# Optimization experiments

Measured on AMD Instinct MI355X. Metric: run time of the kernel, lower is better.

Reference implementation:

```python
import jax, jax.numpy as jnp
import numpy as np

D_MODEL = 1024
NUM_HEADS = 16
D_K = D_MODEL // NUM_HEADS


def setup_inputs() -> dict:
    key = jax.random.key(0)
    ks = jax.random.split(key, 9)
    s = 1.0 / np.sqrt(D_MODEL)
    return {
        "z": jax.random.normal(ks[0], (4, 2048, D_MODEL), dtype=jnp.float32),
        "Wq": jax.random.uniform(ks[1], (D_MODEL, D_MODEL), jnp.float32, -s, s),
        "bq": jax.random.uniform(ks[2], (D_MODEL,), jnp.float32, -s, s),
        "Wk": jax.random.uniform(ks[3], (D_MODEL, D_MODEL), jnp.float32, -s, s),
        "bk": jax.random.uniform(ks[4], (D_MODEL,), jnp.float32, -s, s),
        "Wv": jax.random.uniform(ks[5], (D_MODEL, D_MODEL), jnp.float32, -s, s),
        "bv": jax.random.uniform(ks[6], (D_MODEL,), jnp.float32, -s, s),
        "Wo": jax.random.uniform(ks[7], (D_MODEL, D_MODEL), jnp.float32, -s, s),
        "bo": jax.random.uniform(ks[8], (D_MODEL,), jnp.float32, -s, s),
    }


def reference(z, Wq, bq, Wk, bk, Wv, bv, Wo, bo):
    B, S, _ = z.shape
    # project and split heads: [B, H, S, d_k]
    def proj(W, b):
        return (z @ W.T + b).reshape(B, S, NUM_HEADS, D_K).transpose(0, 2, 1, 3)
    Q, K, V = proj(Wq, bq), proj(Wk, bk), proj(Wv, bv)
    scale = 1.0 / np.sqrt(D_K)
    scores = jnp.einsum('bhqd,bhkd->bhqk', Q, K) * scale
    probs = jax.nn.softmax(scores, axis=-1)
    ctx = jnp.einsum('bhqk,bhkd->bhqd', probs, V)
    ctx = ctx.transpose(0, 2, 1, 3).reshape(B, S, D_MODEL)
    return ctx @ Wo.T + bo
```

## Files before the change

kernel.cpp:

```cpp
#include <hip/hip_runtime.h>
#include <stdint.h>

#define D_MODEL 1024
#define NHEAD 16
#define DKH 64
#define BATCH 4
#define SEQ 2048
#define M_ROWS (BATCH*SEQ)
#define NBH (BATCH*NHEAD)

typedef float f32x4 __attribute__((ext_vector_type(4)));
typedef float f32x16 __attribute__((ext_vector_type(16)));
typedef __bf16 bf16x8 __attribute__((ext_vector_type(8)));
typedef __bf16 bf16x4v __attribute__((ext_vector_type(4)));
typedef short short4v __attribute__((ext_vector_type(4)));
typedef unsigned int uint2v __attribute__((ext_vector_type(2)));

__device__ __forceinline__ unsigned short f2bf(float x) {
    __bf16 b = (__bf16)x;
    return __builtin_bit_cast(unsigned short, b);
}

#define GLL(gsrc, ldst) \
    __builtin_amdgcn_global_load_lds((const __attribute__((address_space(1))) void*)(gsrc), \
                                     (__attribute__((address_space(3))) void*)(ldst), 16, 0, 0)

__global__ __launch_bounds__(256) void k_convert(
    const float* __restrict__ z,  const float* __restrict__ wq,
    const float* __restrict__ wk, const float* __restrict__ wv,
    const float* __restrict__ wo,
    const float* __restrict__ bq, const float* __restrict__ bk,
    const float* __restrict__ bv,
    unsigned short* __restrict__ zb, unsigned short* __restrict__ wqkv,
    unsigned short* __restrict__ wob, float* __restrict__ biasf)
{
    int i = blockIdx.x * 256 + threadIdx.x;
    {
        float4 v = ((const float4*)z)[i];
        ushort4 o; o.x = f2bf(v.x); o.y = f2bf(v.y); o.z = f2bf(v.z); o.w = f2bf(v.w);
        ((ushort4*)zb)[i] = o;
    }
    if (i < 262144) {
        float4 v;
        ushort4 o;
        v = ((const float4*)wq)[i];
        o.x=f2bf(v.x); o.y=f2bf(v.y); o.z=f2bf(v.z); o.w=f2bf(v.w);
        ((ushort4*)wqkv)[i] = o;
        v = ((const float4*)wk)[i];
        o.x=f2bf(v.x); o.y=f2bf(v.y); o.z=f2bf(v.z); o.w=f2bf(v.w);
        ((ushort4*)wqkv)[262144 + i] = o;
        v = ((const float4*)wv)[i];
        o.x=f2bf(v.x); o.y=f2bf(v.y); o.z=f2bf(v.z); o.w=f2bf(v.w);
        ((ushort4*)wqkv)[524288 + i] = o;
        v = ((const float4*)wo)[i];
        o.x=f2bf(v.x); o.y=f2bf(v.y); o.z=f2bf(v.z); o.w=f2bf(v.w);
        ((ushort4*)wob)[i] = o;
    }
    if (i < 1024) {
        biasf[i]        = bq[i];
        biasf[1024 + i] = bk[i];
        biasf[2048 + i] = bv[i];
    }
}

__global__ __launch_bounds__(256) void k_gemm_qkv(
    const unsigned short* __restrict__ A,
    const unsigned short* __restrict__ Bw,
    const float* __restrict__ biasf,
    unsigned short* __restrict__ qb, unsigned short* __restrict__ kb,
    unsigned short* __restrict__ vtb)
{
    __shared__ unsigned short lds_a[128 * 32];
    __shared__ unsigned short lds_b[128 * 32];

    const int NT = 3072 / 128;
    int bid = blockIdx.x;
    int tn = bid % NT, tm = bid / NT;
    int m0 = tm * 128, n0 = tn * 128;
    int tid = threadIdx.x, wid = tid >> 6, lane = tid & 63;
    int wm = wid >> 1, wn = wid & 1;

    f32x4 acc[4][4] = {};

    int srow = lane >> 2;
    int scol = (lane & 3) * 8;

    for (int kt = 0; kt < 32; ++kt) {
        int k0 = kt * 32;
#pragma unroll
        for (int i = 0; i < 2; ++i) {
            int rb = (wid * 2 + i) * 16;
            GLL(A  + (size_t)(m0 + rb + srow) * 1024 + k0 + scol, lds_a + rb * 32);
            GLL(Bw + (size_t)(n0 + rb + srow) * 1024 + k0 + scol, lds_b + rb * 32);
        }
        __syncthreads();
        bf16x8 af[4], bfr[4];
#pragma unroll
        for (int i = 0; i < 4; ++i)
            af[i] = *(const bf16x8*)(lds_a + (wm * 64 + i * 16 + (lane & 15)) * 32 + (lane >> 4) * 8);
#pragma unroll
        for (int j = 0; j < 4; ++j)
            bfr[j] = *(const bf16x8*)(lds_b + (wn * 64 + j * 16 + (lane & 15)) * 32 + (lane >> 4) * 8);
#pragma unroll
        for (int i = 0; i < 4; ++i)
#pragma unroll
            for (int j = 0; j < 4; ++j)
                acc[i][j] = __builtin_amdgcn_mfma_f32_16x16x32_bf16(af[i], bfr[j], acc[i][j], 0, 0, 0);
        __syncthreads();
    }

    const float QSC = 0.18033688011112042f;
    int t = n0 >> 10;
#pragma unroll
    for (int j = 0; j < 4; ++j) {
        int col = n0 + wn * 64 + j * 16 + (lane & 15);
        float bias = biasf[col];
        int d  = col & 1023;
        int h  = d >> 6;
        int dk = d & 63;
#pragma unroll
        for (int i = 0; i < 4; ++i) {
#pragma unroll
            for (int r = 0; r < 4; ++r) {
                int row = m0 + wm * 64 + i * 16 + (lane >> 4) * 4 + r;
                float v = acc[i][j][r] + bias;
                if (t == 0) v *= QSC;
                unsigned short bv16 = f2bf(v);
                int b_ = row >> 11, s_ = row & 2047;
                int bh = b_ * NHEAD + h;
                if (t == 0) {
                    qb[((size_t)bh * SEQ + s_) * DKH + dk] = bv16;
                } else if (t == 1) {
                    int kvblk = s_ >> 6, r64 = s_ & 63;
                    int t32 = r64 >> 5, l5 = r64 & 31;
                    int ds = dk >> 4, hi2 = (dk >> 3) & 1, e = dk & 7;
                    kb[((size_t)(bh * 32 + kvblk)) * 4096 +
                       (t32 * 4 + ds) * 512 + (hi2 * 32 + l5) * 8 + e] = bv16;
                } else {
                    int kvblk = s_ >> 6, kv64 = s_ & 63;
                    int ks = kv64 >> 3, hi2 = (kv64 >> 2) & 1, e = kv64 & 3;
                    int vt = dk >> 5, l5 = dk & 31;
                    vtb[((size_t)(bh * 32 + kvblk)) * 4096 +
                        (vt * 8 + ks) * 256 + (hi2 * 32 + l5) * 4 + e] = bv16;
                }
            }
        }
    }
}


#define ATTN_STEP(LDSK, LDSV, WPREV, WCUR, DO_PV)                                   \
    {                                                                               \
        f32x16 st0 = {}, st1 = {};                                                  \
        __builtin_amdgcn_s_setprio(1);                                              \
        _Pragma("unroll")                                                           \
        for (int ds = 0; ds < 4; ++ds) {                                            \
            bf16x8 kf0 = *(const bf16x8*)(&(LDSK)[(ds) * 512 + lane * 8]);          \
            bf16x8 kf1 = *(const bf16x8*)(&(LDSK)[(4 + ds) * 512 + lane * 8]);      \
            st0 = __builtin_amdgcn_mfma_f32_32x32x16_bf16(kf0, aq[ds], st0, 0, 0, 0); \
            st1 = __builtin_amdgcn_mfma_f32_32x32x16_bf16(kf1, aq[ds], st1, 0, 0, 0); \
            if (DO_PV) {                                                            \
                short4v vf0 = *(const short4v*)(&(LDSV)[(2 * ds) * 256 + lane * 4]);        \
                short4v vf1 = *(const short4v*)(&(LDSV)[(8 + 2 * ds) * 256 + lane * 4]);    \
                oa0 = __builtin_amdgcn_mfma_f32_32x32x8bf16_1k(vf0, WPREV[2 * ds], oa0, 0, 0, 0); \
                oa1 = __builtin_amdgcn_mfma_f32_32x32x8bf16_1k(vf1, WPREV[2 * ds], oa1, 0, 0, 0); \
                short4v vf2 = *(const short4v*)(&(LDSV)[(2 * ds + 1) * 256 + lane * 4]);    \
                short4v vf3 = *(const short4v*)(&(LDSV)[(8 + 2 * ds + 1) * 256 + lane * 4]);\
                oa0 = __builtin_amdgcn_mfma_f32_32x32x8bf16_1k(vf2, WPREV[2 * ds + 1], oa0, 0, 0, 0); \
                oa1 = __builtin_amdgcn_mfma_f32_32x32x8bf16_1k(vf3, WPREV[2 * ds + 1], oa1, 0, 0, 0); \
            }                                                                       \
        }                                                                           \
        __builtin_amdgcn_s_setprio(0);                                              \
        _Pragma("unroll")                                                           \
        for (int ks = 0; ks < 4; ++ks) {                                            \
            {                                                                       \
                float p0 = __builtin_amdgcn_exp2f(st0[4 * ks + 0]);                 \
                float p1 = __builtin_amdgcn_exp2f(st0[4 * ks + 1]);                 \
                float p2 = __builtin_amdgcn_exp2f(st0[4 * ks + 2]);                 \
                float p3 = __builtin_amdgcn_exp2f(st0[4 * ks + 3]);                 \
                lsum += (p0 + p1) + (p2 + p3);                                      \
                bf16x4v pb;                                                         \
                pb[0] = (__bf16)p0; pb[1] = (__bf16)p1; pb[2] = (__bf16)p2; pb[3] = (__bf16)p3; \
                WCUR[ks] = __builtin_bit_cast(short4v, pb);                         \
            }                                                                       \
            {                                                                       \
                float p0 = __builtin_amdgcn_exp2f(st1[4 * ks + 0]);                 \
                float p1 = __builtin_amdgcn_exp2f(st1[4 * ks + 1]);                 \
                float p2 = __builtin_amdgcn_exp2f(st1[4 * ks + 2]);                 \
                float p3 = __builtin_amdgcn_exp2f(st1[4 * ks + 3]);                 \
                lsum += (p0 + p1) + (p2 + p3);                                      \
                bf16x4v pb;                                                         \
                pb[0] = (__bf16)p0; pb[1] = (__bf16)p1; pb[2] = (__bf16)p2; pb[3] = (__bf16)p3; \
                WCUR[4 + ks] = __builtin_bit_cast(short4v, pb);                     \
            }                                                                       \
        }                                                                           \
    }

#define DRAIN_BARRIER()                                         \
    asm volatile("s_waitcnt vmcnt(0)" ::: "memory");            \
    __builtin_amdgcn_sched_barrier(0);                          \
    __builtin_amdgcn_s_barrier();

__global__ __launch_bounds__(512) void k_attn(
    const unsigned short* __restrict__ qg,
    const unsigned short* __restrict__ kb,
    const unsigned short* __restrict__ vtb,
    unsigned short* __restrict__ ctxb)
{
    __shared__ unsigned short lds_k[2][4096];
    __shared__ unsigned short lds_v[2][4096];

    int bid = blockIdx.x;
    int x = bid & 7, li = bid >> 3;
    int bh = x * 8 + (li >> 3);
    int qt = li & 7;

    int tid = threadIdx.x, wid = tid >> 6, lane = tid & 63;
    int lq = lane & 31, hi = lane >> 5;

    bf16x8 aq[4];
    {
        const unsigned short* qp = qg + ((size_t)bh * SEQ + qt * 256 + wid * 32 + lq) * DKH + hi * 8;
#pragma unroll
        for (int d = 0; d < 4; ++d) aq[d] = *(const bf16x8*)(qp + d * 16);
    }

    float lsum = 0.f;
    f32x16 oa0 = {};
    f32x16 oa1 = {};
    short4v wA[8], wB[8];

    const unsigned short* kbase = kb  + (size_t)bh * 32 * 4096;
    const unsigned short* vbase = vtb + (size_t)bh * 32 * 4096;
    int so = wid * 512 + lane * 8;
    unsigned short* ldk0 = &lds_k[0][wid * 512];
    unsigned short* ldk1 = &lds_k[1][wid * 512];
    unsigned short* ldv0 = &lds_v[0][wid * 512];
    unsigned short* ldv1 = &lds_v[1][wid * 512];

    GLL(kbase + so, ldk0);
    DRAIN_BARRIER();

    GLL(kbase + 4096 + so, ldk1);
    GLL(vbase + so, ldv0);
    ATTN_STEP(lds_k[0], lds_v[0], wB, wA, false);
    DRAIN_BARRIER();

    for (int t = 1; t < 31; t += 2) {
        GLL(kbase + (size_t)(t + 1) * 4096 + so, ldk0);
        GLL(vbase + (size_t)t * 4096 + so, ldv1);
        ATTN_STEP(lds_k[1], lds_v[0], wA, wB, true);
        DRAIN_BARRIER();
        if (t + 2 < 32) GLL(kbase + (size_t)(t + 2) * 4096 + so, ldk1);
        GLL(vbase + (size_t)(t + 1) * 4096 + so, ldv0);
        ATTN_STEP(lds_k[0], lds_v[1], wB, wA, true);
        DRAIN_BARRIER();
    }

    GLL(vbase + (size_t)31 * 4096 + so, ldv1);
    ATTN_STEP(lds_k[1], lds_v[0], wA, wB, true);
    DRAIN_BARRIER();

    __builtin_amdgcn_s_setprio(1);
#pragma unroll
    for (int ks = 0; ks < 8; ++ks) {
        short4v vf0 = *(const short4v*)(&lds_v[1][(ks) * 256 + lane * 4]);
        short4v vf1 = *(const short4v*)(&lds_v[1][(8 + ks) * 256 + lane * 4]);
        oa0 = __builtin_amdgcn_mfma_f32_32x32x8bf16_1k(vf0, wB[ks], oa0, 0, 0, 0);
        oa1 = __builtin_amdgcn_mfma_f32_32x32x8bf16_1k(vf1, wB[ks], oa1, 0, 0, 0);
    }
    __builtin_amdgcn_s_setprio(0);

    int b_ = bh >> 4, h = bh & 15;
    lsum += __shfl_xor(lsum, 32);
    float inv = 1.0f / lsum;
    int s_ = qt * 256 + wid * 32 + lq;
    unsigned short* op = ctxb + (((size_t)b_ * SEQ + s_) * NHEAD + h) * DKH;
#pragma unroll
    for (int m = 0; m < 4; ++m) {
        {
            unsigned int u0 = ((unsigned int)f2bf(oa0[4 * m + 1] * inv) << 16) | f2bf(oa0[4 * m + 0] * inv);
            unsigned int u1 = ((unsigned int)f2bf(oa0[4 * m + 3] * inv) << 16) | f2bf(oa0[4 * m + 2] * inv);
            *(uint2v*)(op + 8 * m + 4 * hi) = (uint2v){ u0, u1 };
        }
        {
            unsigned int u0 = ((unsigned int)f2bf(oa1[4 * m + 1] * inv) << 16) | f2bf(oa1[4 * m + 0] * inv);
            unsigned int u1 = ((unsigned int)f2bf(oa1[4 * m + 3] * inv) << 16) | f2bf(oa1[4 * m + 2] * inv);
            *(uint2v*)(op + 32 + 8 * m + 4 * hi) = (uint2v){ u0, u1 };
        }
    }
}

__global__ __launch_bounds__(256) void k_gemm_out(
    const unsigned short* __restrict__ A,
    const unsigned short* __restrict__ Bw,
    const float* __restrict__ bo,
    float* __restrict__ out)
{
    __shared__ unsigned short lds_a[128 * 32];
    __shared__ unsigned short lds_b[128 * 32];

    const int NT = 1024 / 128;
    int bid = blockIdx.x;
    int tn = bid % NT, tm = bid / NT;
    int m0 = tm * 128, n0 = tn * 128;
    int tid = threadIdx.x, wid = tid >> 6, lane = tid & 63;
    int wm = wid >> 1, wn = wid & 1;

    f32x4 acc[4][4] = {};

    int srow = lane >> 2;
    int scol = (lane & 3) * 8;

    for (int kt = 0; kt < 32; ++kt) {
        int k0 = kt * 32;
#pragma unroll
        for (int i = 0; i < 2; ++i) {
            int rb = (wid * 2 + i) * 16;
            GLL(A  + (size_t)(m0 + rb + srow) * 1024 + k0 + scol, lds_a + rb * 32);
            GLL(Bw + (size_t)(n0 + rb + srow) * 1024 + k0 + scol, lds_b + rb * 32);
        }
        __syncthreads();
        bf16x8 af[4], bfr[4];
#pragma unroll
        for (int i = 0; i < 4; ++i)
            af[i] = *(const bf16x8*)(lds_a + (wm * 64 + i * 16 + (lane & 15)) * 32 + (lane >> 4) * 8);
#pragma unroll
        for (int j = 0; j < 4; ++j)
            bfr[j] = *(const bf16x8*)(lds_b + (wn * 64 + j * 16 + (lane & 15)) * 32 + (lane >> 4) * 8);
#pragma unroll
        for (int i = 0; i < 4; ++i)
#pragma unroll
            for (int j = 0; j < 4; ++j)
                acc[i][j] = __builtin_amdgcn_mfma_f32_16x16x32_bf16(af[i], bfr[j], acc[i][j], 0, 0, 0);
        __syncthreads();
    }

#pragma unroll
    for (int j = 0; j < 4; ++j) {
        int col = n0 + wn * 64 + j * 16 + (lane & 15);
        float bias = bo[col];
#pragma unroll
        for (int i = 0; i < 4; ++i) {
#pragma unroll
            for (int r = 0; r < 4; ++r) {
                int row = m0 + wm * 64 + i * 16 + (lane >> 4) * 4 + r;
                out[(size_t)row * 1024 + col] = acc[i][j][r] + bias;
            }
        }
    }
}

extern "C" void kernel_launch(void* const* d_in, const int* in_sizes, int n_in,
                              void* d_out, int out_size, void* d_ws, size_t ws_size,
                              hipStream_t stream)
{
    const float* z  = (const float*)d_in[0];
    const float* Wq = (const float*)d_in[1];
    const float* bq = (const float*)d_in[2];
    const float* Wk = (const float*)d_in[3];
    const float* bk = (const float*)d_in[4];
    const float* Wv = (const float*)d_in[5];
    const float* bv = (const float*)d_in[6];
    const float* Wo = (const float*)d_in[7];
    const float* bo = (const float*)d_in[8];
    float* out = (float*)d_out;

    char* ws = (char*)d_ws;
    unsigned short* zb   = (unsigned short*)(ws);
    unsigned short* ctxb = (unsigned short*)(ws);
    unsigned short* wqkv = (unsigned short*)(ws + (16ull << 20));
    unsigned short* wob  = (unsigned short*)(ws + (22ull << 20));
    float*          biasf= (float*)(ws + (24ull << 20));
    unsigned short* qb   = (unsigned short*)(ws + (25ull << 20));
    unsigned short* kb   = (unsigned short*)(ws + (41ull << 20));
    unsigned short* vtb  = (unsigned short*)(ws + (57ull << 20));

    k_convert<<<8192, 256, 0, stream>>>(z, Wq, Wk, Wv, Wo, bq, bk, bv, zb, wqkv, wob, biasf);
    k_gemm_qkv<<<64 * 24, 256, 0, stream>>>(zb, wqkv, biasf, qb, kb, vtb);
    k_attn<<<NBH * 8, 512, 0, stream>>>(qb, kb, vtb, ctxb);
    k_gemm_out<<<64 * 8, 256, 0, stream>>>(ctxb, wob, bo, out);
}
```

Measured before the change: 223.3 us.

## Rewrite GEMMs with fragment-packed operands, 256x128 tiles and triple-buffered LDS pipeline

The convert kernel now writes z, the QKV weights and Wo in an MFMA-fragment-ordered layout, and the attention kernel writes its context output in the same layout. Both GEMMs switch to 512-thread blocks with 256x128 tiles and K-steps of 64. They use a three-stage LDS ring fed by global_load_lds with explicit vmcnt waits, plus a block-index swizzle for L2 locality. The goal is to hide global-load latency, drop a barrier per step and raise MFMA density, at the cost of more LDS (144KB) and therefore lower occupancy.

```diff
diff --git a/kernel.cpp b/kernel.cpp
--- a/kernel.cpp
+++ b/kernel.cpp
@@ -14,6 +14,8 @@
 typedef __bf16 bf16x8 __attribute__((ext_vector_type(8)));
 typedef __bf16 bf16x4v __attribute__((ext_vector_type(4)));
 typedef short short4v __attribute__((ext_vector_type(4)));
+typedef unsigned short ushort4v __attribute__((ext_vector_type(4)));
+typedef unsigned short ushort8v __attribute__((ext_vector_type(8)));
 typedef unsigned int uint2v __attribute__((ext_vector_type(2)));
 
 __device__ __forceinline__ unsigned short f2bf(float x) {
@@ -24,6 +26,17 @@
 #define GLL(gsrc, ldst) \
     __builtin_amdgcn_global_load_lds((const __attribute__((address_space(1))) void*)(gsrc), \
                                      (__attribute__((address_space(3))) void*)(ldst), 16, 0, 0)
+
+
+__device__ __forceinline__ void cvt8store(const float* __restrict__ src,
+                                          unsigned short* __restrict__ dst) {
+    float4 v0 = *(const float4*)(src);
+    float4 v1 = *(const float4*)(src + 4);
+    ushort8v o;
+    o[0] = f2bf(v0.x); o[1] = f2bf(v0.y); o[2] = f2bf(v0.z); o[3] = f2bf(v0.w);
+    o[4] = f2bf(v1.x); o[5] = f2bf(v1.y); o[6] = f2bf(v1.z); o[7] = f2bf(v1.w);
+    *(ushort8v*)dst = o;
+}
 
 __global__ __launch_bounds__(256) void k_convert(
     const float* __restrict__ z,  const float* __restrict__ wq,
@@ -31,30 +44,36 @@
     const float* __restrict__ wo,
     const float* __restrict__ bq, const float* __restrict__ bk,
     const float* __restrict__ bv,
-    unsigned short* __restrict__ zb, unsigned short* __restrict__ wqkv,
-    unsigned short* __restrict__ wob, float* __restrict__ biasf)
+    unsigned short* __restrict__ zf, unsigned short* __restrict__ wqkvf,
+    unsigned short* __restrict__ wobf, float* __restrict__ biasf)
 {
     int i = blockIdx.x * 256 + threadIdx.x;
-    {
-        float4 v = ((const float4*)z)[i];
-        ushort4 o; o.x = f2bf(v.x); o.y = f2bf(v.y); o.z = f2bf(v.z); o.w = f2bf(v.w);
-        ((ushort4*)zb)[i] = o;
-    }
-    if (i < 262144) {
-        float4 v;
-        ushort4 o;
-        v = ((const float4*)wq)[i];
-        o.x=f2bf(v.x); o.y=f2bf(v.y); o.z=f2bf(v.z); o.w=f2bf(v.w);
-        ((ushort4*)wqkv)[i] = o;
-        v = ((const float4*)wk)[i];
-        o.x=f2bf(v.x); o.y=f2bf(v.y); o.z=f2bf(v.z); o.w=f2bf(v.w);
-        ((ushort4*)wqkv)[262144 + i] = o;
-        v = ((const float4*)wv)[i];
-        o.x=f2bf(v.x); o.y=f2bf(v.y); o.z=f2bf(v.z); o.w=f2bf(v.w);
-        ((ushort4*)wqkv)[524288 + i] = o;
-        v = ((const float4*)wo)[i];
-        o.x=f2bf(v.x); o.y=f2bf(v.y); o.z=f2bf(v.z); o.w=f2bf(v.w);
-        ((ushort4*)wob)[i] = o;
+    if (i < 1048576) {
+        int lane = i & 63, rest = i >> 6;
+        int kk = rest & 1, mfrag = (rest >> 1) & 7, half = (rest >> 4) & 1;
+        int kt = (rest >> 5) & 15, mtile = rest >> 9;
+        int row = mtile * 256 + half * 128 + mfrag * 16 + (lane & 15);
+        int k = kt * 64 + kk * 32 + (lane >> 4) * 8;
+        cvt8store(z + (size_t)row * 1024 + k, zf + (size_t)i * 8);
+    }
+    int i2 = i - 1048576;
+    if (i2 >= 0 && i2 < 393216) {
+        int lane = i2 & 63, rest = i2 >> 6;
+        int kk = rest & 1, nfrag = (rest >> 1) & 7;
+        int kt = (rest >> 4) & 15, ntile = rest >> 8;
+        int n = ntile * 128 + nfrag * 16 + (lane & 15);
+        int k = kt * 64 + kk * 32 + (lane >> 4) * 8;
+        const float* W = (n < 1024) ? wq : ((n < 2048) ? wk : wv);
+        cvt8store(W + (size_t)(n & 1023) * 1024 + k, wqkvf + (size_t)i2 * 8);
+    }
+    int i3 = i2 - 393216;
+    if (i3 >= 0 && i3 < 131072) {
+        int lane = i3 & 63, rest = i3 >> 6;
+        int kk = rest & 1, nfrag = (rest >> 1) & 7;
+        int kt = (rest >> 4) & 15, ntile = rest >> 8;
+        int n = ntile * 128 + nfrag * 16 + (lane & 15);
+        int k = kt * 64 + kk * 32 + (lane >> 4) * 8;
+        cvt8store(wo + (size_t)n * 1024 + k, wobf + (size_t)i3 * 8);
     }
     if (i < 1024) {
         biasf[i]        = bq[i];
@@ -63,91 +82,107 @@
     }
 }
 
-__global__ __launch_bounds__(256) void k_gemm_qkv(
-    const unsigned short* __restrict__ A,
-    const unsigned short* __restrict__ Bw,
+__device__ __forceinline__ void g_stage(const unsigned short* __restrict__ as_,
+                                        const unsigned short* __restrict__ bs_,
+                                        unsigned short* la, unsigned short* lb,
+                                        int wid, int lane)
+{
+#pragma unroll
+    for (int g = 0; g < 4; ++g)
+        GLL(as_ + (wid + 8 * g) * 512 + lane * 8, la + (wid + 8 * g) * 512);
+#pragma unroll
+    for (int g = 0; g < 2; ++g)
+        GLL(bs_ + (wid + 8 * g) * 512 + lane * 8, lb + (wid + 8 * g) * 512);
+}
+
+#define GEMM_KLOOP(Abase, Bbase)                                                      \
+    g_stage(Abase, Bbase, &ldsA[0][0], &ldsB[0][0], wid, lane);                       \
+    g_stage(Abase + 16384, Bbase + 8192, &ldsA[1][0], &ldsB[1][0], wid, lane);        \
+    asm volatile("s_waitcnt vmcnt(6)" ::: "memory");                                  \
+    __builtin_amdgcn_s_barrier();                                                     \
+    for (int t = 0; t < 16; ++t) {                                                    \
+        int buf = t % 3;                                                              \
+        if (t + 2 < 16)                                                               \
+            g_stage(Abase + (size_t)(t + 2) * 16384, Bbase + (size_t)(t + 2) * 8192,  \
+                    &ldsA[(t + 2) % 3][0], &ldsB[(t + 2) % 3][0], wid, lane);         \
+        const unsigned short* A = &ldsA[buf][0];                                      \
+        const unsigned short* B = &ldsB[buf][0];                                      \
+        bf16x8 b00 = *(const bf16x8*)(B + ((wn * 2 + 0) * 2 + 0) * 512 + lane * 8);   \
+        bf16x8 b01 = *(const bf16x8*)(B + ((wn * 2 + 0) * 2 + 1) * 512 + lane * 8);   \
+        bf16x8 b10 = *(const bf16x8*)(B + ((wn * 2 + 1) * 2 + 0) * 512 + lane * 8);   \
+        bf16x8 b11 = *(const bf16x8*)(B + ((wn * 2 + 1) * 2 + 1) * 512 + lane * 8);   \
+        _Pragma("unroll")                                                             \
+        for (int ii = 0; ii < 8; ++ii) {                                              \
+            bf16x8 a0 = *(const bf16x8*)(A + ((wm * 8 + ii) * 2 + 0) * 512 + lane * 8); \
+            bf16x8 a1 = *(const bf16x8*)(A + ((wm * 8 + ii) * 2 + 1) * 512 + lane * 8); \
+            acc[ii][0] = __builtin_amdgcn_mfma_f32_16x16x32_bf16(a0, b00, acc[ii][0], 0, 0, 0); \
+            acc[ii][0] = __builtin_amdgcn_mfma_f32_16x16x32_bf16(a1, b01, acc[ii][0], 0, 0, 0); \
+            acc[ii][1] = __builtin_amdgcn_mfma_f32_16x16x32_bf16(a0, b10, acc[ii][1], 0, 0, 0); \
+            acc[ii][1] = __builtin_amdgcn_mfma_f32_16x16x32_bf16(a1, b11, acc[ii][1], 0, 0, 0); \
+        }                                                                             \
+        if (t < 14)       { asm volatile("s_waitcnt vmcnt(6)" ::: "memory"); }        \
+        else if (t == 14) { asm volatile("s_waitcnt vmcnt(0)" ::: "memory"); }        \
+        if (t < 15) { __builtin_amdgcn_sched_barrier(0); __builtin_amdgcn_s_barrier(); } \
+    }
+
+__global__ __launch_bounds__(512) void k_gemm_qkv(
+    const unsigned short* __restrict__ Af,
+    const unsigned short* __restrict__ Bf,
     const float* __restrict__ biasf,
-    unsigned short* __restrict__ qb, unsigned short* __restrict__ kb,
-    unsigned short* __restrict__ vtb)
-{
-    __shared__ unsigned short lds_a[128 * 32];
-    __shared__ unsigned short lds_b[128 * 32];
-
-    const int NT = 3072 / 128;
+    unsigned short* __restrict__ qb, unsigned short* __restrict__ kfrag,
+    unsigned short* __restrict__ vfrag)
+{
+    __shared__ unsigned short ldsA[3][16384];
+    __shared__ unsigned short ldsB[3][8192];
+
     int bid = blockIdx.x;
-    int tn = bid % NT, tm = bid / NT;
-    int m0 = tm * 128, n0 = tn * 128;
+    int wg = (bid & 7) * 96 + (bid >> 3);
+    int tn = wg % 24, tm = wg / 24;
     int tid = threadIdx.x, wid = tid >> 6, lane = tid & 63;
-    int wm = wid >> 1, wn = wid & 1;
-
-    f32x4 acc[4][4] = {};
-
-    int srow = lane >> 2;
-    int scol = (lane & 3) * 8;
-
-    for (int kt = 0; kt < 32; ++kt) {
-        int k0 = kt * 32;
-#pragma unroll
-        for (int i = 0; i < 2; ++i) {
-            int rb = (wid * 2 + i) * 16;
-            GLL(A  + (size_t)(m0 + rb + srow) * 1024 + k0 + scol, lds_a + rb * 32);
-            GLL(Bw + (size_t)(n0 + rb + srow) * 1024 + k0 + scol, lds_b + rb * 32);
-        }
-        __syncthreads();
-        bf16x8 af[4], bfr[4];
-#pragma unroll
-        for (int i = 0; i < 4; ++i)
-            af[i] = *(const bf16x8*)(lds_a + (wm * 64 + i * 16 + (lane & 15)) * 32 + (lane >> 4) * 8);
-#pragma unroll
-        for (int j = 0; j < 4; ++j)
-            bfr[j] = *(const bf16x8*)(lds_b + (wn * 64 + j * 16 + (lane & 15)) * 32 + (lane >> 4) * 8);
-#pragma unroll
-        for (int i = 0; i < 4; ++i)
-#pragma unroll
-            for (int j = 0; j < 4; ++j)
-                acc[i][j] = __builtin_amdgcn_mfma_f32_16x16x32_bf16(af[i], bfr[j], acc[i][j], 0, 0, 0);
-        __syncthreads();
-    }
+    int wm = wid >> 2, wn = wid & 3;
+
+    const unsigned short* Abase = Af + (size_t)tm * 16 * 16384;
+    const unsigned short* Bbase = Bf + (size_t)tn * 16 * 8192;
+
+    f32x4 acc[8][2] = {};
+    GEMM_KLOOP(Abase, Bbase)
 
     const float QSC = 0.18033688011112042f;
-    int t = n0 >> 10;
-#pragma unroll
-    for (int j = 0; j < 4; ++j) {
-        int col = n0 + wn * 64 + j * 16 + (lane & 15);
+    int t3 = tn >> 3;
+#pragma unroll
+    for (int j = 0; j < 2; ++j) {
+        int col = tn * 128 + wn * 32 + j * 16 + (lane & 15);
         float bias = biasf[col];
-        int d  = col & 1023;
-        int h  = d >> 6;
-        int dk = d & 63;
-#pragma unroll
-        for (int i = 0; i < 4; ++i) {
+        int d = col & 1023, h = d >> 6, dk = d & 63;
+#pragma unroll
+        for (int i = 0; i < 8; ++i) {
 #pragma unroll
             for (int r = 0; r < 4; ++r) {
-                int row = m0 + wm * 64 + i * 16 + (lane >> 4) * 4 + r;
+                int row = tm * 256 + wm * 128 + i * 16 + (lane >> 4) * 4 + r;
                 float v = acc[i][j][r] + bias;
-                if (t == 0) v *= QSC;
+                if (t3 == 0) v *= QSC;
                 unsigned short bv16 = f2bf(v);
                 int b_ = row >> 11, s_ = row & 2047;
                 int bh = b_ * NHEAD + h;
-                if (t == 0) {
+                if (t3 == 0) {
                     qb[((size_t)bh * SEQ + s_) * DKH + dk] = bv16;
-                } else if (t == 1) {
+                } else if (t3 == 1) {
                     int kvblk = s_ >> 6, r64 = s_ & 63;
                     int t32 = r64 >> 5, l5 = r64 & 31;
                     int ds = dk >> 4, hi2 = (dk >> 3) & 1, e = dk & 7;
-                    kb[((size_t)(bh * 32 + kvblk)) * 4096 +
-                       (t32 * 4 + ds) * 512 + (hi2 * 32 + l5) * 8 + e] = bv16;
+                    kfrag[((size_t)(bh * 32 + kvblk)) * 4096 +
+                          (t32 * 4 + ds) * 512 + (hi2 * 32 + l5) * 8 + e] = bv16;
                 } else {
                     int kvblk = s_ >> 6, kv64 = s_ & 63;
                     int ks = kv64 >> 3, hi2 = (kv64 >> 2) & 1, e = kv64 & 3;
                     int vt = dk >> 5, l5 = dk & 31;
-                    vtb[((size_t)(bh * 32 + kvblk)) * 4096 +
-                        (vt * 8 + ks) * 256 + (hi2 * 32 + l5) * 4 + e] = bv16;
+                    vfrag[((size_t)(bh * 32 + kvblk)) * 4096 +
+                          (vt * 8 + ks) * 256 + (hi2 * 32 + l5) * 4 + e] = bv16;
                 }
             }
         }
     }
 }
-
 
 #define ATTN_STEP(LDSK, LDSV, WPREV, WCUR, DO_PV)                                   \
     {                                                                               \
@@ -205,7 +240,7 @@
     const unsigned short* __restrict__ qg,
     const unsigned short* __restrict__ kb,
     const unsigned short* __restrict__ vtb,
-    unsigned short* __restrict__ ctxb)
+    unsigned short* __restrict__ ctxf)
 {
     __shared__ unsigned short lds_k[2][4096];
     __shared__ unsigned short lds_v[2][4096];
@@ -275,76 +310,52 @@
     lsum += __shfl_xor(lsum, 32);
     float inv = 1.0f / lsum;
     int s_ = qt * 256 + wid * 32 + lq;
-    unsigned short* op = ctxb + (((size_t)b_ * SEQ + s_) * NHEAD + h) * DKH;
+    int row = b_ * 2048 + s_;
+    int mtile = row >> 8, half = (row >> 7) & 1, mfrag = (row >> 4) & 7, lrow = row & 15;
+    unsigned short* cb = ctxf + (size_t)((mtile * 16 + h) * 2 + half) * 8192
+                              + mfrag * 1024 + lrow * 8 + 4 * hi;
 #pragma unroll
     for (int m = 0; m < 4; ++m) {
-        {
-            unsigned int u0 = ((unsigned int)f2bf(oa0[4 * m + 1] * inv) << 16) | f2bf(oa0[4 * m + 0] * inv);
-            unsigned int u1 = ((unsigned int)f2bf(oa0[4 * m + 3] * inv) << 16) | f2bf(oa0[4 * m + 2] * inv);
-            *(uint2v*)(op + 8 * m + 4 * hi) = (uint2v){ u0, u1 };
-        }
-        {
-            unsigned int u0 = ((unsigned int)f2bf(oa1[4 * m + 1] * inv) << 16) | f2bf(oa1[4 * m + 0] * inv);
-            unsigned int u1 = ((unsigned int)f2bf(oa1[4 * m + 3] * inv) << 16) | f2bf(oa1[4 * m + 2] * inv);
-            *(uint2v*)(op + 32 + 8 * m + 4 * hi) = (uint2v){ u0, u1 };
-        }
-    }
-}
-
-__global__ __launch_bounds__(256) void k_gemm_out(
-    const unsigned short* __restrict__ A,
-    const unsigned short* __restrict__ Bw,
+        ushort4v s0, s1;
+        s0[0] = f2bf(oa0[4 * m + 0] * inv); s0[1] = f2bf(oa0[4 * m + 1] * inv);
+        s0[2] = f2bf(oa0[4 * m + 2] * inv); s0[3] = f2bf(oa0[4 * m + 3] * inv);
+        *(ushort4v*)(cb + m * 128) = s0;
+        s1[0] = f2bf(oa1[4 * m + 0] * inv); s1[1] = f2bf(oa1[4 * m + 1] * inv);
+        s1[2] = f2bf(oa1[4 * m + 2] * inv); s1[3] = f2bf(oa1[4 * m + 3] * inv);
+        *(ushort4v*)(cb + 512 + m * 128) = s1;
+    }
+}
+
+__global__ __launch_bounds__(512) void k_gemm_out(
+    const unsigned short* __restrict__ Af,
+    const unsigned short* __restrict__ Bf,
     const float* __restrict__ bo,
     float* __restrict__ out)
 {
-    __shared__ unsigned short lds_a[128 * 32];
-    __shared__ unsigned short lds_b[128 * 32];
-
-    const int NT = 1024 / 128;
+    __shared__ unsigned short ldsA[3][16384];
+    __shared__ unsigned short ldsB[3][8192];
+
     int bid = blockIdx.x;
-    int tn = bid % NT, tm = bid / NT;
-    int m0 = tm * 128, n0 = tn * 128;
+    int wg = (bid & 7) * 32 + (bid >> 3);
+    int tn = wg % 8, tm = wg / 8;
     int tid = threadIdx.x, wid = tid >> 6, lane = tid & 63;
-    int wm = wid >> 1, wn = wid & 1;
-
-    f32x4 acc[4][4] = {};
-
-    int srow = lane >> 2;
-    int scol = (lane & 3) * 8;
-
-    for (int kt = 0; kt < 32; ++kt) {
-        int k0 = kt * 32;
-#pragma unroll
-        for (int i = 0; i < 2; ++i) {
-            int rb = (wid * 2 + i) * 16;
-            GLL(A  + (size_t)(m0 + rb + srow) * 1024 + k0 + scol, lds_a + rb * 32);
-            GLL(Bw + (size_t)(n0 + rb + srow) * 1024 + k0 + scol, lds_b + rb * 32);
-        }
-        __syncthreads();
-        bf16x8 af[4], bfr[4];
-#pragma unroll
-        for (int i = 0; i < 4; ++i)
-            af[i] = *(const bf16x8*)(lds_a + (wm * 64 + i * 16 + (lane & 15)) * 32 + (lane >> 4) * 8);
-#pragma unroll
-        for (int j = 0; j < 4; ++j)
-            bfr[j] = *(const bf16x8*)(lds_b + (wn * 64 + j * 16 + (lane & 15)) * 32 + (lane >> 4) * 8);
-#pragma unroll
-        for (int i = 0; i < 4; ++i)
-#pragma unroll
-            for (int j = 0; j < 4; ++j)
-                acc[i][j] = __builtin_amdgcn_mfma_f32_16x16x32_bf16(af[i], bfr[j], acc[i][j], 0, 0, 0);
-        __syncthreads();
-    }
-
-#pragma unroll
-    for (int j = 0; j < 4; ++j) {
-        int col = n0 + wn * 64 + j * 16 + (lane & 15);
+    int wm = wid >> 2, wn = wid & 3;
+
+    const unsigned short* Abase = Af + (size_t)tm * 16 * 16384;
+    const unsigned short* Bbase = Bf + (size_t)tn * 16 * 8192;
+
+    f32x4 acc[8][2] = {};
+    GEMM_KLOOP(Abase, Bbase)
+
+#pragma unroll
+    for (int j = 0; j < 2; ++j) {
+        int col = tn * 128 + wn * 32 + j * 16 + (lane & 15);
         float bias = bo[col];
 #pragma unroll
-        for (int i = 0; i < 4; ++i) {
+        for (int i = 0; i < 8; ++i) {
 #pragma unroll
             for (int r = 0; r < 4; ++r) {
-                int row = m0 + wm * 64 + i * 16 + (lane >> 4) * 4 + r;
+                int row = tm * 256 + wm * 128 + i * 16 + (lane >> 4) * 4 + r;
                 out[(size_t)row * 1024 + col] = acc[i][j][r] + bias;
             }
         }
@@ -367,17 +378,17 @@
     float* out = (float*)d_out;
 
     char* ws = (char*)d_ws;
-    unsigned short* zb   = (unsigned short*)(ws);
-    unsigned short* ctxb = (unsigned short*)(ws);
-    unsigned short* wqkv = (unsigned short*)(ws + (16ull << 20));
-    unsigned short* wob  = (unsigned short*)(ws + (22ull << 20));
-    float*          biasf= (float*)(ws + (24ull << 20));
-    unsigned short* qb   = (unsigned short*)(ws + (25ull << 20));
-    unsigned short* kb   = (unsigned short*)(ws + (41ull << 20));
-    unsigned short* vtb  = (unsigned short*)(ws + (57ull << 20));
-
-    k_convert<<<8192, 256, 0, stream>>>(z, Wq, Wk, Wv, Wo, bq, bk, bv, zb, wqkv, wob, biasf);
-    k_gemm_qkv<<<64 * 24, 256, 0, stream>>>(zb, wqkv, biasf, qb, kb, vtb);
-    k_attn<<<NBH * 8, 512, 0, stream>>>(qb, kb, vtb, ctxb);
-    k_gemm_out<<<64 * 8, 256, 0, stream>>>(ctxb, wob, bo, out);
-}
+    unsigned short* zf    = (unsigned short*)(ws);
+    unsigned short* ctxf  = (unsigned short*)(ws);
+    unsigned short* wqkvf = (unsigned short*)(ws + (16ull << 20));
+    unsigned short* wobf  = (unsigned short*)(ws + (22ull << 20));
+    float*          biasf = (float*)(ws + (24ull << 20));
+    unsigned short* qb    = (unsigned short*)(ws + (25ull << 20));
+    unsigned short* kfrag = (unsigned short*)(ws + (41ull << 20));
+    unsigned short* vfrag = (unsigned short*)(ws + (57ull << 20));
+
+    k_convert<<<8192, 256, 0, stream>>>(z, Wq, Wk, Wv, Wo, bq, bk, bv, zf, wqkvf, wobf, biasf);
+    k_gemm_qkv<<<768, 512, 0, stream>>>(zf, wqkvf, biasf, qb, kfrag, vfrag);
+    k_attn<<<NBH * 8, 512, 0, stream>>>(qb, kfrag, vfrag, ctxf);
+    k_gemm_out<<<256, 512, 0, stream>>>(ctxf, wobf, bo, out);
+}
```

Result: faster. 214.2 us (-4.1%).
